# Performance work log

Measured on AMD Instinct MI355X. Metric: run time of the kernel, lower is better.

The kernel has to match this reference:

```python
import jax, jax.numpy as jnp
import numpy as np

N_NODES = 100_000
N_EDGES = 800_000
D_IN = 64
HID = 32   # hidden_channels
OUT = 64   # out_channels
H1, H2, H3 = 7, 4, 1


def _lin(key, din, dout, scale=0.05):
    k1, k2 = jax.random.split(key)
    W = jax.random.normal(k1, (din, dout), jnp.float32) * scale
    b = jax.random.normal(k2, (dout,), jnp.float32) * scale
    return W, b


def setup_inputs() -> dict:
    key = jax.random.key(0)
    ks = jax.random.split(key, 16)
    x = jax.random.normal(ks[0], (N_NODES, D_IN), jnp.float32)
    edge_index = jax.random.randint(ks[1], (2, N_EDGES), 0, N_NODES, dtype=jnp.int32)
    inp = {"x": x, "edge_index": edge_index}
    # (in_dim, heads, per-head channels) for the 3 TransformerConv layers
    dims = [(D_IN, H1, HID), (H1 * HID, H2, HID), (H2 * HID, H3, OUT)]
    i = 2
    for l, (din, h, c) in enumerate(dims, start=1):
        for nm in ("q", "k", "v", "s"):  # query, key, value, skip linears
            W, b = _lin(ks[i], din, h * c)
            i += 1
            inp[f"W{nm}{l}"] = W
            inp[f"b{nm}{l}"] = b
    return inp


def _transformer_conv(x, src, dst, Wq, bq, Wk, bk, Wv, bv, Ws, bs, H, C):
    # PyG TransformerConv (concat=True, beta=False, root_weight=True, no edge feats)
    q = (x @ Wq + bq).reshape(-1, H, C)
    k = (x @ Wk + bk).reshape(-1, H, C)
    v = (x @ Wv + bv).reshape(-1, H, C)
    # per-edge attention logits [E, H]
    alpha = jnp.einsum('ehc,ehc->eh', q[dst], k[src]) / jnp.sqrt(jnp.asarray(C, q.dtype))
    # segment softmax over incoming edges of each dst node
    amax = jax.ops.segment_max(alpha, dst, num_segments=N_NODES)
    ex = jnp.exp(alpha - amax[dst])
    denom = jax.ops.segment_sum(ex, dst, num_segments=N_NODES)
    attn = ex / (denom[dst] + 1e-16)
    # weighted message aggregation [N, H, C] -> [N, H*C]
    msg = v[src] * attn[..., None]
    out = jax.ops.segment_sum(msg, dst, num_segments=N_NODES).reshape(N_NODES, H * C)
    # root/skip connection
    return out + x @ Ws + bs


def reference(x, edge_index,
              Wq1, bq1, Wk1, bk1, Wv1, bv1, Ws1, bs1,
              Wq2, bq2, Wk2, bk2, Wv2, bv2, Ws2, bs2,
              Wq3, bq3, Wk3, bk3, Wv3, bv3, Ws3, bs3):
    src, dst = edge_index[0], edge_index[1]
    h = jax.nn.relu(_transformer_conv(x, src, dst, Wq1, bq1, Wk1, bk1, Wv1, bv1, Ws1, bs1, H1, HID))
    h = jax.nn.relu(_transformer_conv(h, src, dst, Wq2, bq2, Wk2, bk2, Wv2, bv2, Ws2, bs2, H2, HID))
    return _transformer_conv(h, src, dst, Wq3, bq3, Wk3, bk3, Wv3, bv3, Ws3, bs3, H3, OUT)
```

## Files before the change

kernel.cpp:

```cpp
#include <hip/hip_runtime.h>
#include <hip/hip_bf16.h>
#include <math.h>

#define N_NODES 100000
#define N_EDGES 800000
#define SCAN_BLOCKS 98

typedef __attribute__((ext_vector_type(8))) short short8;
typedef __attribute__((ext_vector_type(4))) float f32x4;

__device__ __forceinline__ unsigned short f2b(float f) {
    __hip_bfloat16 h = __float2bfloat16(f);
    return *reinterpret_cast<unsigned short*>(&h);
}
__device__ __forceinline__ float2 up2(unsigned u) {
    unsigned lo = u << 16;
    unsigned hi = u & 0xffff0000u;
    float2 r;
    __builtin_memcpy(&r.x, &lo, 4);
    __builtin_memcpy(&r.y, &hi, 4);
    return r;
}
__device__ __forceinline__ float dot4(float2 qa, float2 qb, unsigned k0, unsigned k1) {
    float2 x = up2(k0), y = up2(k1);
    float p = x.x * qa.x;
    p = fmaf(x.y, qa.y, p);
    p = fmaf(y.x, qb.x, p);
    p = fmaf(y.y, qb.y, p);
    return p;
}


__global__ void hist_kernel(const int* __restrict__ dst, int* __restrict__ deg) {
    int e = blockIdx.x * blockDim.x + threadIdx.x;
    if (e < N_EDGES) atomicAdd(&deg[dst[e]], 1);
}

__global__ __launch_bounds__(1024) void scan_part(const int* __restrict__ deg,
                                                  int* __restrict__ rowptr,
                                                  int* __restrict__ partials) {
    __shared__ int buf[1024];
    const int t = threadIdx.x;
    const int i = blockIdx.x * 1024 + t;
    int x = (i < N_NODES) ? deg[i] : 0;
    buf[t] = x;
    __syncthreads();
    for (int off = 1; off < 1024; off <<= 1) {
        int y = (t >= off) ? buf[t - off] : 0;
        __syncthreads();
        buf[t] += y;
        __syncthreads();
    }
    if (i < N_NODES) rowptr[i] = buf[t] - x;
    if (t == 1023) partials[blockIdx.x] = buf[t];
}

__global__ __launch_bounds__(128) void scan_tail(int* __restrict__ partials,
                                                 int* __restrict__ rowptr) {
    __shared__ int buf[128];
    const int t = threadIdx.x;
    int x = (t < SCAN_BLOCKS) ? partials[t] : 0;
    buf[t] = x;
    __syncthreads();
    for (int off = 1; off < 128; off <<= 1) {
        int y = (t >= off) ? buf[t - off] : 0;
        __syncthreads();
        buf[t] += y;
        __syncthreads();
    }
    if (t < SCAN_BLOCKS) partials[t] = buf[t] - x;
    if (t == 127) rowptr[N_NODES] = buf[127];
}

__global__ __launch_bounds__(1024) void scan_add(int* __restrict__ rowptr,
                                                 const int* __restrict__ partials) {
    const int i = blockIdx.x * 1024 + threadIdx.x;
    if (i < N_NODES) rowptr[i] += partials[blockIdx.x];
}

__global__ void scatter_kernel(const int* __restrict__ src, const int* __restrict__ dst,
                               const int* __restrict__ rowptr, int* __restrict__ cursor,
                               int* __restrict__ sorted_src) {
    int e = blockIdx.x * blockDim.x + threadIdx.x;
    if (e < N_EDGES) {
        int d = dst[e];
        int pos = atomicAdd(&cursor[d], 1);
        sorted_src[rowptr[d] + pos] = src[e];
    }
}

__global__ void fill_kernel(float* __restrict__ out, int n, float val) {
    int i = blockIdx.x * blockDim.x + threadIdx.x;
    if (i < n) out[i] = val;
}


__global__ void convert_kernel(const float* __restrict__ X, unsigned short* __restrict__ Y, int n4) {
    int i = blockIdx.x * blockDim.x + threadIdx.x;
    if (i < n4) {
        float4 f = ((const float4*)X)[i];
        ushort4 u;
        u.x = f2b(f.x); u.y = f2b(f.y); u.z = f2b(f.z); u.w = f2b(f.w);
        ((ushort4*)Y)[i] = u;
    }
}

__global__ void build_wt(const float* __restrict__ Wq, const float* __restrict__ Wk,
                         const float* __restrict__ Wv, const float* __restrict__ Wsk,
                         const float* __restrict__ bq, const float* __restrict__ bk,
                         const float* __restrict__ bv, const float* __restrict__ bsk,
                         unsigned short* __restrict__ WT, float* __restrict__ biasF,
                         int K, int HC, int C) {
    int total = 4 * HC * K;
    int idx = blockIdx.x * blockDim.x + threadIdx.x;
    if (idx >= total) return;
    int rowc = idx / K;
    int kk = idx - rowc * K;
    const float* W;
    const float* Bp;
    int cw;
    if (rowc < HC) {
        W = Wq; Bp = bq; cw = rowc;
    } else if (rowc < 3 * HC) {
        int u = rowc - HC;
        int h = u / (2 * C);
        int rr = u - h * 2 * C;
        int grp = rr >> 3, w = rr & 7;
        if (w < 4) { W = Wk;  Bp = bk;  cw = h * C + grp * 4 + w; }
        else       { W = Wv;  Bp = bv;  cw = h * C + grp * 4 + w - 4; }
    } else {
        W = Wsk; Bp = bsk; cw = rowc - 3 * HC;
    }
    WT[idx] = f2b(W[(size_t)kk * HC + cw]);
    if (kk == 0) biasF[rowc] = Bp[cw];
}


template <int K, bool YBF>
__global__ __launch_bounds__(256) void mfma_gemm(
    const unsigned short* __restrict__ Xb, const unsigned short* __restrict__ WT,
    const float* __restrict__ biasF, void* __restrict__ Y,
    int ncols, int ostride, int split, int rq, int rkv) {
    constexpr int STR = 40;
    constexpr int ESTR = 136;
    __shared__ __align__(16) char smem[128 * ESTR * 2];
    unsigned short* Xs = (unsigned short*)smem;
    unsigned short* Ws = (unsigned short*)(smem + 128 * STR * 2);
    const int t = threadIdx.x;
    const int wave = t >> 6, lane = t & 63, quad = lane >> 4, l16 = lane & 15;
    const int n0 = blockIdx.x * 128, c0 = blockIdx.y * 128;

    f32x4 acc[2][8];
#pragma unroll
    for (int i = 0; i < 2; ++i)
#pragma unroll
        for (int j = 0; j < 8; ++j)
#pragma unroll
            for (int r = 0; r < 4; ++r) acc[i][j][r] = 0.f;

    for (int k0 = 0; k0 < K; k0 += 32) {
#pragma unroll
        for (int i = 0; i < 2; ++i) {
            int idx = t + i * 256;
            int row = idx >> 2;
            int seg = (idx & 3) << 3;
            int gr = n0 + row;
            short8 xv;
#pragma unroll
            for (int z = 0; z < 8; ++z) xv[z] = 0;
            if (gr < N_NODES)
                xv = *(const short8*)(Xb + (size_t)gr * K + k0 + seg);
            *(short8*)(&Xs[row * STR + seg]) = xv;

            int c = c0 + row;
            short8 wv;
#pragma unroll
            for (int z = 0; z < 8; ++z) wv[z] = 0;
            if (c < ncols) {
                int wtrow = (c < split) ? (rq + c) : (rkv + (c - split));
                wv = *(const short8*)(WT + (size_t)wtrow * K + k0 + seg);
            }
            *(short8*)(&Ws[row * STR + seg]) = wv;
        }
        __syncthreads();

        short8 af0 = *(short8*)(&Xs[(wave * 32 + l16) * STR + quad * 8]);
        short8 af1 = *(short8*)(&Xs[(wave * 32 + 16 + l16) * STR + quad * 8]);
#pragma unroll
        for (int ct = 0; ct < 8; ++ct) {
            short8 bfr = *(short8*)(&Ws[(ct * 16 + l16) * STR + quad * 8]);
            acc[0][ct] = __builtin_amdgcn_mfma_f32_16x16x32_bf16(af0, bfr, acc[0][ct], 0, 0, 0);
            acc[1][ct] = __builtin_amdgcn_mfma_f32_16x16x32_bf16(af1, bfr, acc[1][ct], 0, 0, 0);
        }
        __syncthreads();
    }

    if constexpr (YBF) {
        unsigned short* Es = (unsigned short*)smem;
#pragma unroll
        for (int ct = 0; ct < 8; ++ct) {
            if (c0 + ct * 16 >= ncols) break;
            int col = c0 + ct * 16 + l16;
            int brow = (col < split) ? (rq + col) : (rkv + (col - split));
            float bv = biasF[brow];
#pragma unroll
            for (int rt = 0; rt < 2; ++rt)
#pragma unroll
                for (int r = 0; r < 4; ++r) {
                    int row = wave * 32 + rt * 16 + quad * 4 + r;
                    Es[row * ESTR + ct * 16 + l16] = f2b(acc[rt][ct][r] + bv);
                }
        }
        __syncthreads();
        const int erow = t >> 1;
        const int cb = (t & 1) * 8;
        const int gr = n0 + erow;
#pragma unroll
        for (int j = 0; j < 8; ++j) {
            int gc = c0 + j * 16 + cb;
            if (gr < N_NODES && gc < ncols)
                *(short8*)((unsigned short*)Y + (size_t)gr * ostride + gc) =
                    *(const short8*)(&Es[erow * ESTR + j * 16 + cb]);
        }
    } else {
#pragma unroll
        for (int ct = 0; ct < 8; ++ct) {
            int col = c0 + ct * 16 + l16;
            if (col >= ncols) continue;
            int brow = (col < split) ? (rq + col) : (rkv + (col - split));
            float bv = biasF[brow];
#pragma unroll
            for (int rt = 0; rt < 2; ++rt) {
#pragma unroll
                for (int r = 0; r < 4; ++r) {
                    int row = n0 + wave * 32 + rt * 16 + quad * 4 + r;
                    if (row < N_NODES)
                        ((float*)Y)[(size_t)row * ostride + col] = acc[rt][ct][r] + bv;
                }
            }
        }
    }
}

template <int K, bool YBF>
static inline void launch_gemm(const unsigned short* Xb, const unsigned short* WT,
                               const float* biasF, void* Y, int ncols, int ostride,
                               int split, int rq, int rkv, hipStream_t s) {
    const int GX = (N_NODES + 127) / 128;
    int ny = (ncols + 127) / 128;
    mfma_gemm<K, YBF><<<dim3(GX, ny), 256, 0, s>>>(
        Xb, WT, biasF, Y, ncols, ostride, split, rq, rkv);
}


template <int C, int NH, bool RELU, bool YBF>
__global__ __launch_bounds__(256) void attn3(
    const unsigned short* __restrict__ F,
    const int* __restrict__ rowptr, const int* __restrict__ ssrc,
    void* __restrict__ Hv, int h0, int ostride) {
    constexpr int LPN = NH * C / 4;
    constexpr int NPW = 64 / LPN;
    constexpr int gC = NH * C;
    constexpr int Ms = 3 * gC;
    const int lane = threadIdx.x & 63;
    const int wave = (blockIdx.x * 256 + threadIdx.x) >> 6;
    const int slot = lane / LPN;
    const int cl = lane - slot * LPN;
    const int n = wave * NPW + slot;
    if (slot >= NPW || n >= N_NODES) return;

    const int head = cl / (C / 4);
    const int c4 = (cl - head * (C / 4)) * 4;
    const int qoff = head * C + c4;
    const int kvoff = gC + head * 2 * C + 2 * c4;
    const float SCALE2 = ((C == 64) ? 0.125f : 0.17677669529663687f) * 1.44269504f;

    uint2 qu = *(const uint2*)(F + (size_t)n * Ms + qoff);
    float2 qa = up2(qu.x), qb = up2(qu.y);
    qa.x *= SCALE2; qa.y *= SCALE2; qb.x *= SCALE2; qb.y *= SCALE2;
    int s0 = rowptr[n], s1 = rowptr[n + 1];

    float l = 0.f, a0 = 0.f, a1 = 0.f, a2 = 0.f, a3 = 0.f;
    int ei = s0;
    for (; ei + 3 < s1; ei += 4) {
        int iA = ssrc[ei], iB = ssrc[ei + 1], iC = ssrc[ei + 2], iD = ssrc[ei + 3];
        uint4 A = *(const uint4*)(F + (size_t)iA * Ms + kvoff);
        uint4 B = *(const uint4*)(F + (size_t)iB * Ms + kvoff);
        uint4 Cv = *(const uint4*)(F + (size_t)iC * Ms + kvoff);
        uint4 D = *(const uint4*)(F + (size_t)iD * Ms + kvoff);
        float pA = dot4(qa, qb, A.x, A.y);
        float pB = dot4(qa, qb, B.x, B.y);
        float pC = dot4(qa, qb, Cv.x, Cv.y);
        float pD = dot4(qa, qb, D.x, D.y);
#pragma unroll
        for (int off = C / 8; off > 0; off >>= 1) {
            pA += __shfl_xor(pA, off);
            pB += __shfl_xor(pB, off);
            pC += __shfl_xor(pC, off);
            pD += __shfl_xor(pD, off);
        }
        float eA = exp2f(pA), eB = exp2f(pB), eC = exp2f(pC), eD = exp2f(pD);
        l += (eA + eB) + (eC + eD);
        float2 vA0 = up2(A.z), vA1 = up2(A.w);
        float2 vB0 = up2(B.z), vB1 = up2(B.w);
        float2 vC0 = up2(Cv.z), vC1 = up2(Cv.w);
        float2 vD0 = up2(D.z), vD1 = up2(D.w);
        a0 = fmaf(eA, vA0.x, fmaf(eB, vB0.x, fmaf(eC, vC0.x, fmaf(eD, vD0.x, a0))));
        a1 = fmaf(eA, vA0.y, fmaf(eB, vB0.y, fmaf(eC, vC0.y, fmaf(eD, vD0.y, a1))));
        a2 = fmaf(eA, vA1.x, fmaf(eB, vB1.x, fmaf(eC, vC1.x, fmaf(eD, vD1.x, a2))));
        a3 = fmaf(eA, vA1.y, fmaf(eB, vB1.y, fmaf(eC, vC1.y, fmaf(eD, vD1.y, a3))));
    }
    if (ei + 1 < s1) {
        int iA = ssrc[ei], iB = ssrc[ei + 1];
        ei += 2;
        uint4 A = *(const uint4*)(F + (size_t)iA * Ms + kvoff);
        uint4 B = *(const uint4*)(F + (size_t)iB * Ms + kvoff);
        float pA = dot4(qa, qb, A.x, A.y);
        float pB = dot4(qa, qb, B.x, B.y);
#pragma unroll
        for (int off = C / 8; off > 0; off >>= 1) {
            pA += __shfl_xor(pA, off);
            pB += __shfl_xor(pB, off);
        }
        float eA = exp2f(pA), eB = exp2f(pB);
        l += eA + eB;
        float2 vA0 = up2(A.z), vA1 = up2(A.w);
        float2 vB0 = up2(B.z), vB1 = up2(B.w);
        a0 = fmaf(eA, vA0.x, fmaf(eB, vB0.x, a0));
        a1 = fmaf(eA, vA0.y, fmaf(eB, vB0.y, a1));
        a2 = fmaf(eA, vA1.x, fmaf(eB, vB1.x, a2));
        a3 = fmaf(eA, vA1.y, fmaf(eB, vB1.y, a3));
    }
    if (ei < s1) {
        int iA = ssrc[ei];
        uint4 A = *(const uint4*)(F + (size_t)iA * Ms + kvoff);
        float pA = dot4(qa, qb, A.x, A.y);
#pragma unroll
        for (int off = C / 8; off > 0; off >>= 1) pA += __shfl_xor(pA, off);
        float eA = exp2f(pA);
        l += eA;
        float2 vA0 = up2(A.z), vA1 = up2(A.w);
        a0 = fmaf(eA, vA0.x, a0);
        a1 = fmaf(eA, vA0.y, a1);
        a2 = fmaf(eA, vA1.x, a2);
        a3 = fmaf(eA, vA1.y, a3);
    }

    float inv = 1.f / (l + 1e-16f);
    float r0 = a0 * inv, r1 = a1 * inv, r2 = a2 * inv, r3 = a3 * inv;

    const int col = (h0 + head) * C + c4;
    if constexpr (YBF) {
        uint2* Hp = (uint2*)((unsigned short*)Hv + (size_t)n * ostride + col);
        uint2 hv = *Hp;
        float2 hx = up2(hv.x), hy = up2(hv.y);
        float o0 = hx.x + r0, o1 = hx.y + r1, o2 = hy.x + r2, o3 = hy.y + r3;
        if (RELU) {
            o0 = fmaxf(o0, 0.f); o1 = fmaxf(o1, 0.f);
            o2 = fmaxf(o2, 0.f); o3 = fmaxf(o3, 0.f);
        }
        uint2 pv;
        pv.x = (unsigned)f2b(o0) | ((unsigned)f2b(o1) << 16);
        pv.y = (unsigned)f2b(o2) | ((unsigned)f2b(o3) << 16);
        *Hp = pv;
    } else {
        float4* Hp = (float4*)((float*)Hv + (size_t)n * ostride + col);
        float4 h = *Hp;
        h.x += r0; h.y += r1; h.z += r2; h.w += r3;
        if (RELU) {
            h.x = fmaxf(h.x, 0.f); h.y = fmaxf(h.y, 0.f);
            h.z = fmaxf(h.z, 0.f); h.w = fmaxf(h.w, 0.f);
        }
        *Hp = h;
    }
}

static inline void launch_attn32(int NH, int h0, const unsigned short* F,
                                 void* H, int ostride, const int* rowptr,
                                 const int* ssrc, hipStream_t stream) {
    switch (NH) {
        case 1: attn3<32, 1, true, true><<<3125, 256, 0, stream>>>(F, rowptr, ssrc, H, h0, ostride); break;
        case 2: attn3<32, 2, true, true><<<6250, 256, 0, stream>>>(F, rowptr, ssrc, H, h0, ostride); break;
        case 3: attn3<32, 3, true, true><<<12500, 256, 0, stream>>>(F, rowptr, ssrc, H, h0, ostride); break;
        case 4: attn3<32, 4, true, true><<<12500, 256, 0, stream>>>(F, rowptr, ssrc, H, h0, ostride); break;
        default: attn3<32, 7, true, true><<<25000, 256, 0, stream>>>(F, rowptr, ssrc, H, h0, ostride); break;
    }
}


extern "C" void kernel_launch(void* const* d_in, const int* in_sizes, int n_in,
                              void* d_out, int out_size, void* d_ws, size_t ws_size,
                              hipStream_t stream) {
    const float* x = (const float*)d_in[0];
    const int* ei = (const int*)d_in[1];
    const int* srcp = ei;
    const int* dstp = ei + N_EDGES;

    const float* W[12];
    const float* B[12];
    for (int i = 0; i < 12; ++i) {
        W[i] = (const float*)d_in[2 + 2 * i];
        B[i] = (const float*)d_in[3 + 2 * i];
    }
    float* out = (float*)d_out;

    char* p = (char*)d_ws;
    size_t off = 0;
    unsigned short* wt  = (unsigned short*)(p + off); off += 240000;
    float* biasF        = (float*)(p + off);          off += 4096;
    int* rowptr = (int*)(p + off); off += sizeof(int) * (N_NODES + 1);
    int* deg    = (int*)(p + off); off += sizeof(int) * N_NODES;
    int* cursor = (int*)(p + off); off += sizeof(int) * N_NODES;
    int* partials = (int*)(p + off); off += sizeof(int) * 128;
    int* ssrc   = (int*)(p + off); off += sizeof(int) * N_EDGES;
    off = (off + 255) & ~(size_t)255;
    unsigned short* h1  = (unsigned short*)(p + off); off += (size_t)224 * N_NODES * 2;
    unsigned short* h2  = (unsigned short*)(p + off); off += (size_t)128 * N_NODES * 2;
    unsigned short* xb1 = (unsigned short*)(p + off); off += (size_t)64 * N_NODES * 2;
    unsigned short* tail = (unsigned short*)(p + off);

    if (ws_size < off + 6500000) {
        fill_kernel<<<(out_size + 255) / 256, 256, 0, stream>>>(out, out_size, (float)(ws_size >> 20));
        return;
    }
    size_t tail_bytes = ws_size - off;
    const size_t F1PASS = (size_t)3 * 32 * N_NODES * 2;

    int nh1[7], np1 = 0;
    int nh2[4], np2 = 0;
    unsigned short *F1w, *F2w;
    if (tail_bytes >= 7 * F1PASS) {
        nh1[np1++] = 7;
        nh2[np2++] = 4;
        F1w = F2w = tail;
    } else if (tail_bytes >= 4 * F1PASS) {
        nh1[np1++] = 4; nh1[np1++] = 3;
        nh2[np2++] = 4;
        F1w = F2w = tail;
    } else if (tail_bytes >= 2 * F1PASS) {
        nh1[np1++] = 2; nh1[np1++] = 2; nh1[np1++] = 2; nh1[np1++] = 1;
        nh2[np2++] = 2; nh2[np2++] = 2;
        F1w = F2w = tail;
    } else {
        for (int i = 0; i < 7; ++i) nh1[np1++] = 1;
        for (int i = 0; i < 4; ++i) nh2[np2++] = 1;
        F1w = h2;
        F2w = xb1;
    }
    unsigned short* F3 = h1;

    hipMemsetAsync(deg, 0, sizeof(int) * 2 * N_NODES, stream);
    hist_kernel<<<(N_EDGES + 255) / 256, 256, 0, stream>>>(dstp, deg);
    scan_part<<<SCAN_BLOCKS, 1024, 0, stream>>>(deg, rowptr, partials);
    scan_tail<<<1, 128, 0, stream>>>(partials, rowptr);
    scan_add<<<SCAN_BLOCKS, 1024, 0, stream>>>(rowptr, partials);
    scatter_kernel<<<(N_EDGES + 255) / 256, 256, 0, stream>>>(srcp, dstp, rowptr, cursor, ssrc);

    convert_kernel<<<(N_NODES * 64 / 4 + 255) / 256, 256, 0, stream>>>(x, xb1, N_NODES * 64 / 4);

    build_wt<<<(4 * 224 * 64 + 255) / 256, 256, 0, stream>>>(
        W[0], W[1], W[2], W[3], B[0], B[1], B[2], B[3], wt, biasF, 64, 224, 32);
    launch_gemm<64, true>(xb1, wt + (size_t)3 * 224 * 64, biasF + 3 * 224, h1,
                          224, 224, 224, 0, 0, stream);
    {
        int h0 = 0;
        for (int pass = 0; pass < np1; ++pass) {
            int NH = nh1[pass];
            int nc = 3 * NH * 32;
            launch_gemm<64, true>(xb1, wt, biasF, F1w, nc, nc,
                                  NH * 32, h0 * 32,
                                  224 + 2 * h0 * 32, stream);
            launch_attn32(NH, h0, F1w, h1, 224, rowptr, ssrc, stream);
            h0 += NH;
        }
    }

    build_wt<<<(4 * 128 * 224 + 255) / 256, 256, 0, stream>>>(
        W[4], W[5], W[6], W[7], B[4], B[5], B[6], B[7], wt, biasF, 224, 128, 32);
    launch_gemm<224, true>(h1, wt + (size_t)3 * 128 * 224, biasF + 3 * 128, h2,
                           128, 128, 128, 0, 0, stream);
    {
        int h0 = 0;
        for (int pass = 0; pass < np2; ++pass) {
            int NH = nh2[pass];
            int nc = 3 * NH * 32;
            launch_gemm<224, true>(h1, wt, biasF, F2w, nc, nc,
                                   NH * 32, h0 * 32,
                                   128 + 2 * h0 * 32, stream);
            launch_attn32(NH, h0, F2w, h2, 128, rowptr, ssrc, stream);
            h0 += NH;
        }
    }

    build_wt<<<(4 * 64 * 128 + 255) / 256, 256, 0, stream>>>(
        W[8], W[9], W[10], W[11], B[8], B[9], B[10], B[11], wt, biasF, 128, 64, 64);
    launch_gemm<128, true>(h2, wt, biasF, F3, 192, 192,
                           64, 0, 64, stream);
    launch_gemm<128, false>(h2, wt + (size_t)3 * 64 * 128, biasF + 3 * 64, out,
                            64, 64, 64, 0, 0, stream);
    attn3<64, 1, false, false><<<6250, 256, 0, stream>>>(F3, rowptr, ssrc, out, 0, 64);
}
```

Baseline: 665.5 us.

## Store attention keys in FP8 and split K from Q/V layout for layers 1-2

For the first two TransformerConv layers, keys are now written as FP8 e4m3 through a separate GEMM epilogue into their own buffer, and Q/V stay bf16 in a narrower [Q|V] layout. The attention kernel gathers 4-byte FP8 key chunks and 8-byte bf16 value chunks per edge instead of one 16-byte interleaved K/V chunk. This cuts the gather traffic in the memory-bound edge loop. The cost is an extra GEMM launch that recomputes the X tile per pass, two separate gathers per edge, and reduced key precision that may hurt accuracy.

New measurement: 664.9 us. No clear change (-0.1%).

```diff
diff --git a/kernel.cpp b/kernel.cpp
--- a/kernel.cpp
+++ b/kernel.cpp
@@ -1,5 +1,6 @@
 #include <hip/hip_runtime.h>
 #include <hip/hip_bf16.h>
+#include <hip/hip_fp8.h>
 #include <math.h>
 
 #define N_NODES 100000
@@ -8,6 +9,7 @@
 
 typedef __attribute__((ext_vector_type(8))) short short8;
 typedef __attribute__((ext_vector_type(4))) float f32x4;
+typedef __attribute__((ext_vector_type(2))) float f32x2;
 
 __device__ __forceinline__ unsigned short f2b(float f) {
     __hip_bfloat16 h = __float2bfloat16(f);
@@ -20,6 +22,37 @@
     __builtin_memcpy(&r.x, &lo, 4);
     __builtin_memcpy(&r.y, &hi, 4);
     return r;
+}
+__device__ __forceinline__ unsigned char f2fp8(float f) {
+#if __has_builtin(__builtin_amdgcn_cvt_pk_fp8_f32)
+    unsigned u = __builtin_amdgcn_cvt_pk_fp8_f32(f, f, 0u, false);
+    return (unsigned char)(u & 0xffu);
+#else
+    __hip_fp8_e4m3 h(f);
+    return (unsigned char)h.__x;
+#endif
+}
+__device__ __forceinline__ float dotk(float2 qa, float2 qb, unsigned k4) {
+#if __has_builtin(__builtin_amdgcn_cvt_pk_f32_fp8)
+    f32x2 lo = __builtin_amdgcn_cvt_pk_f32_fp8(k4, false);
+    f32x2 hi = __builtin_amdgcn_cvt_pk_f32_fp8(k4, true);
+    float p = lo[0] * qa.x;
+    p = fmaf(lo[1], qa.y, p);
+    p = fmaf(hi[0], qb.x, p);
+    p = fmaf(hi[1], qb.y, p);
+    return p;
+#else
+    __hip_fp8_e4m3 a, b, c, d;
+    a.__x = (unsigned char)k4;
+    b.__x = (unsigned char)(k4 >> 8);
+    c.__x = (unsigned char)(k4 >> 16);
+    d.__x = (unsigned char)(k4 >> 24);
+    float p = (float)a * qa.x;
+    p = fmaf((float)b, qa.y, p);
+    p = fmaf((float)c, qb.x, p);
+    p = fmaf((float)d, qb.y, p);
+    return p;
+#endif
 }
 __device__ __forceinline__ float dot4(float2 qa, float2 qb, unsigned k0, unsigned k1) {
     float2 x = up2(k0), y = up2(k1);
@@ -110,7 +143,7 @@
                          const float* __restrict__ bq, const float* __restrict__ bk,
                          const float* __restrict__ bv, const float* __restrict__ bsk,
                          unsigned short* __restrict__ WT, float* __restrict__ biasF,
-                         int K, int HC, int C) {
+                         int K, int HC, int C, int mode) {
     int total = 4 * HC * K;
     int idx = blockIdx.x * blockDim.x + threadIdx.x;
     if (idx >= total) return;
@@ -119,24 +152,31 @@
     const float* W;
     const float* Bp;
     int cw;
-    if (rowc < HC) {
-        W = Wq; Bp = bq; cw = rowc;
-    } else if (rowc < 3 * HC) {
-        int u = rowc - HC;
-        int h = u / (2 * C);
-        int rr = u - h * 2 * C;
-        int grp = rr >> 3, w = rr & 7;
-        if (w < 4) { W = Wk;  Bp = bk;  cw = h * C + grp * 4 + w; }
-        else       { W = Wv;  Bp = bv;  cw = h * C + grp * 4 + w - 4; }
+    if (mode == 0) {
+        if (rowc < HC)          { W = Wq;  Bp = bq;  cw = rowc; }
+        else if (rowc < 2 * HC) { W = Wv;  Bp = bv;  cw = rowc - HC; }
+        else if (rowc < 3 * HC) { W = Wk;  Bp = bk;  cw = rowc - 2 * HC; }
+        else                    { W = Wsk; Bp = bsk; cw = rowc - 3 * HC; }
     } else {
-        W = Wsk; Bp = bsk; cw = rowc - 3 * HC;
+        if (rowc < HC) {
+            W = Wq; Bp = bq; cw = rowc;
+        } else if (rowc < 3 * HC) {
+            int u = rowc - HC;
+            int h = u / (2 * C);
+            int rr = u - h * 2 * C;
+            int grp = rr >> 3, w = rr & 7;
+            if (w < 4) { W = Wk; Bp = bk; cw = h * C + grp * 4 + w; }
+            else       { W = Wv; Bp = bv; cw = h * C + grp * 4 + w - 4; }
+        } else {
+            W = Wsk; Bp = bsk; cw = rowc - 3 * HC;
+        }
     }
     WT[idx] = f2b(W[(size_t)kk * HC + cw]);
     if (kk == 0) biasF[rowc] = Bp[cw];
 }
 
 
-template <int K, bool YBF>
+template <int K, int YMODE>
 __global__ __launch_bounds__(256) void mfma_gemm(
     const unsigned short* __restrict__ Xb, const unsigned short* __restrict__ WT,
     const float* __restrict__ biasF, void* __restrict__ Y,
@@ -195,7 +235,7 @@
         __syncthreads();
     }
 
-    if constexpr (YBF) {
+    if constexpr (YMODE == 1) {
         unsigned short* Es = (unsigned short*)smem;
 #pragma unroll
         for (int ct = 0; ct < 8; ++ct) {
@@ -221,6 +261,34 @@
             if (gr < N_NODES && gc < ncols)
                 *(short8*)((unsigned short*)Y + (size_t)gr * ostride + gc) =
                     *(const short8*)(&Es[erow * ESTR + j * 16 + cb]);
+        }
+    } else if constexpr (YMODE == 2) {
+        constexpr int EB = 144;
+        unsigned char* Es = (unsigned char*)smem;
+#pragma unroll
+        for (int ct = 0; ct < 8; ++ct) {
+            if (c0 + ct * 16 >= ncols) break;
+            int col = c0 + ct * 16 + l16;
+            int brow = (col < split) ? (rq + col) : (rkv + (col - split));
+            float bv = biasF[brow];
+#pragma unroll
+            for (int rt = 0; rt < 2; ++rt)
+#pragma unroll
+                for (int r = 0; r < 4; ++r) {
+                    int row = wave * 32 + rt * 16 + quad * 4 + r;
+                    Es[row * EB + ct * 16 + l16] = f2fp8(acc[rt][ct][r] + bv);
+                }
+        }
+        __syncthreads();
+        const int erow = t >> 1;
+        const int q8 = (t & 1) * 64;
+        const int gr = n0 + erow;
+#pragma unroll
+        for (int j = 0; j < 4; ++j) {
+            int gc = c0 + q8 + j * 16;
+            if (gr < N_NODES && gc < ncols)
+                *(uint4*)((unsigned char*)Y + (size_t)gr * ostride + gc) =
+                    *(const uint4*)(&Es[erow * EB + q8 + j * 16]);
         }
     } else {
 #pragma unroll
@@ -242,26 +310,26 @@
     }
 }
 
-template <int K, bool YBF>
+template <int K, int YMODE>
 static inline void launch_gemm(const unsigned short* Xb, const unsigned short* WT,
                                const float* biasF, void* Y, int ncols, int ostride,
                                int split, int rq, int rkv, hipStream_t s) {
     const int GX = (N_NODES + 127) / 128;
     int ny = (ncols + 127) / 128;
-    mfma_gemm<K, YBF><<<dim3(GX, ny), 256, 0, s>>>(
+    mfma_gemm<K, YMODE><<<dim3(GX, ny), 256, 0, s>>>(
         Xb, WT, biasF, Y, ncols, ostride, split, rq, rkv);
 }
 
 
-template <int C, int NH, bool RELU, bool YBF>
+template <int C, int NH, bool RELU, bool YBF, bool KF8>
 __global__ __launch_bounds__(256) void attn3(
-    const unsigned short* __restrict__ F,
+    const unsigned short* __restrict__ F, const unsigned char* __restrict__ K8,
     const int* __restrict__ rowptr, const int* __restrict__ ssrc,
     void* __restrict__ Hv, int h0, int ostride) {
     constexpr int LPN = NH * C / 4;
     constexpr int NPW = 64 / LPN;
     constexpr int gC = NH * C;
-    constexpr int Ms = 3 * gC;
+    constexpr int Ms = KF8 ? (2 * gC) : (3 * gC);
     const int lane = threadIdx.x & 63;
     const int wave = (blockIdx.x * 256 + threadIdx.x) >> 6;
     const int slot = lane / LPN;
@@ -272,6 +340,7 @@
     const int head = cl / (C / 4);
     const int c4 = (cl - head * (C / 4)) * 4;
     const int qoff = head * C + c4;
+    const int voff = gC + qoff;
     const int kvoff = gC + head * 2 * C + 2 * c4;
     const float SCALE2 = ((C == 64) ? 0.125f : 0.17677669529663687f) * 1.44269504f;
 
@@ -282,68 +351,141 @@
 
     float l = 0.f, a0 = 0.f, a1 = 0.f, a2 = 0.f, a3 = 0.f;
     int ei = s0;
-    for (; ei + 3 < s1; ei += 4) {
-        int iA = ssrc[ei], iB = ssrc[ei + 1], iC = ssrc[ei + 2], iD = ssrc[ei + 3];
-        uint4 A = *(const uint4*)(F + (size_t)iA * Ms + kvoff);
-        uint4 B = *(const uint4*)(F + (size_t)iB * Ms + kvoff);
-        uint4 Cv = *(const uint4*)(F + (size_t)iC * Ms + kvoff);
-        uint4 D = *(const uint4*)(F + (size_t)iD * Ms + kvoff);
-        float pA = dot4(qa, qb, A.x, A.y);
-        float pB = dot4(qa, qb, B.x, B.y);
-        float pC = dot4(qa, qb, Cv.x, Cv.y);
-        float pD = dot4(qa, qb, D.x, D.y);
-#pragma unroll
-        for (int off = C / 8; off > 0; off >>= 1) {
-            pA += __shfl_xor(pA, off);
-            pB += __shfl_xor(pB, off);
-            pC += __shfl_xor(pC, off);
-            pD += __shfl_xor(pD, off);
-        }
-        float eA = exp2f(pA), eB = exp2f(pB), eC = exp2f(pC), eD = exp2f(pD);
-        l += (eA + eB) + (eC + eD);
-        float2 vA0 = up2(A.z), vA1 = up2(A.w);
-        float2 vB0 = up2(B.z), vB1 = up2(B.w);
-        float2 vC0 = up2(Cv.z), vC1 = up2(Cv.w);
-        float2 vD0 = up2(D.z), vD1 = up2(D.w);
-        a0 = fmaf(eA, vA0.x, fmaf(eB, vB0.x, fmaf(eC, vC0.x, fmaf(eD, vD0.x, a0))));
-        a1 = fmaf(eA, vA0.y, fmaf(eB, vB0.y, fmaf(eC, vC0.y, fmaf(eD, vD0.y, a1))));
-        a2 = fmaf(eA, vA1.x, fmaf(eB, vB1.x, fmaf(eC, vC1.x, fmaf(eD, vD1.x, a2))));
-        a3 = fmaf(eA, vA1.y, fmaf(eB, vB1.y, fmaf(eC, vC1.y, fmaf(eD, vD1.y, a3))));
-    }
-    if (ei + 1 < s1) {
-        int iA = ssrc[ei], iB = ssrc[ei + 1];
-        ei += 2;
-        uint4 A = *(const uint4*)(F + (size_t)iA * Ms + kvoff);
-        uint4 B = *(const uint4*)(F + (size_t)iB * Ms + kvoff);
-        float pA = dot4(qa, qb, A.x, A.y);
-        float pB = dot4(qa, qb, B.x, B.y);
-#pragma unroll
-        for (int off = C / 8; off > 0; off >>= 1) {
-            pA += __shfl_xor(pA, off);
-            pB += __shfl_xor(pB, off);
-        }
-        float eA = exp2f(pA), eB = exp2f(pB);
-        l += eA + eB;
-        float2 vA0 = up2(A.z), vA1 = up2(A.w);
-        float2 vB0 = up2(B.z), vB1 = up2(B.w);
-        a0 = fmaf(eA, vA0.x, fmaf(eB, vB0.x, a0));
-        a1 = fmaf(eA, vA0.y, fmaf(eB, vB0.y, a1));
-        a2 = fmaf(eA, vA1.x, fmaf(eB, vB1.x, a2));
-        a3 = fmaf(eA, vA1.y, fmaf(eB, vB1.y, a3));
-    }
-    if (ei < s1) {
-        int iA = ssrc[ei];
-        uint4 A = *(const uint4*)(F + (size_t)iA * Ms + kvoff);
-        float pA = dot4(qa, qb, A.x, A.y);
-#pragma unroll
-        for (int off = C / 8; off > 0; off >>= 1) pA += __shfl_xor(pA, off);
-        float eA = exp2f(pA);
-        l += eA;
-        float2 vA0 = up2(A.z), vA1 = up2(A.w);
-        a0 = fmaf(eA, vA0.x, a0);
-        a1 = fmaf(eA, vA0.y, a1);
-        a2 = fmaf(eA, vA1.x, a2);
-        a3 = fmaf(eA, vA1.y, a3);
+    if constexpr (KF8) {
+        for (; ei + 3 < s1; ei += 4) {
+            int iA = ssrc[ei], iB = ssrc[ei + 1], iC = ssrc[ei + 2], iD = ssrc[ei + 3];
+            unsigned kA = *(const unsigned*)(K8 + (size_t)iA * gC + qoff);
+            unsigned kB = *(const unsigned*)(K8 + (size_t)iB * gC + qoff);
+            unsigned kC = *(const unsigned*)(K8 + (size_t)iC * gC + qoff);
+            unsigned kD = *(const unsigned*)(K8 + (size_t)iD * gC + qoff);
+            uint2 vAu = *(const uint2*)(F + (size_t)iA * Ms + voff);
+            uint2 vBu = *(const uint2*)(F + (size_t)iB * Ms + voff);
+            uint2 vCu = *(const uint2*)(F + (size_t)iC * Ms + voff);
+            uint2 vDu = *(const uint2*)(F + (size_t)iD * Ms + voff);
+            float pA = dotk(qa, qb, kA);
+            float pB = dotk(qa, qb, kB);
+            float pC = dotk(qa, qb, kC);
+            float pD = dotk(qa, qb, kD);
+#pragma unroll
+            for (int off = C / 8; off > 0; off >>= 1) {
+                pA += __shfl_xor(pA, off);
+                pB += __shfl_xor(pB, off);
+                pC += __shfl_xor(pC, off);
+                pD += __shfl_xor(pD, off);
+            }
+            float eA = exp2f(pA), eB = exp2f(pB), eC = exp2f(pC), eD = exp2f(pD);
+            l += (eA + eB) + (eC + eD);
+            float2 vA0 = up2(vAu.x), vA1 = up2(vAu.y);
+            float2 vB0 = up2(vBu.x), vB1 = up2(vBu.y);
+            float2 vC0 = up2(vCu.x), vC1 = up2(vCu.y);
+            float2 vD0 = up2(vDu.x), vD1 = up2(vDu.y);
+            a0 = fmaf(eA, vA0.x, fmaf(eB, vB0.x, fmaf(eC, vC0.x, fmaf(eD, vD0.x, a0))));
+            a1 = fmaf(eA, vA0.y, fmaf(eB, vB0.y, fmaf(eC, vC0.y, fmaf(eD, vD0.y, a1))));
+            a2 = fmaf(eA, vA1.x, fmaf(eB, vB1.x, fmaf(eC, vC1.x, fmaf(eD, vD1.x, a2))));
+            a3 = fmaf(eA, vA1.y, fmaf(eB, vB1.y, fmaf(eC, vC1.y, fmaf(eD, vD1.y, a3))));
+        }
+        if (ei + 1 < s1) {
+            int iA = ssrc[ei], iB = ssrc[ei + 1];
+            ei += 2;
+            unsigned kA = *(const unsigned*)(K8 + (size_t)iA * gC + qoff);
+            unsigned kB = *(const unsigned*)(K8 + (size_t)iB * gC + qoff);
+            uint2 vAu = *(const uint2*)(F + (size_t)iA * Ms + voff);
+            uint2 vBu = *(const uint2*)(F + (size_t)iB * Ms + voff);
+            float pA = dotk(qa, qb, kA);
+            float pB = dotk(qa, qb, kB);
+#pragma unroll
+            for (int off = C / 8; off > 0; off >>= 1) {
+                pA += __shfl_xor(pA, off);
+                pB += __shfl_xor(pB, off);
+            }
+            float eA = exp2f(pA), eB = exp2f(pB);
+            l += eA + eB;
+            float2 vA0 = up2(vAu.x), vA1 = up2(vAu.y);
+            float2 vB0 = up2(vBu.x), vB1 = up2(vBu.y);
+            a0 = fmaf(eA, vA0.x, fmaf(eB, vB0.x, a0));
+            a1 = fmaf(eA, vA0.y, fmaf(eB, vB0.y, a1));
+            a2 = fmaf(eA, vA1.x, fmaf(eB, vB1.x, a2));
+            a3 = fmaf(eA, vA1.y, fmaf(eB, vB1.y, a3));
+        }
+        if (ei < s1) {
+            int iA = ssrc[ei];
+            unsigned kA = *(const unsigned*)(K8 + (size_t)iA * gC + qoff);
+            uint2 vAu = *(const uint2*)(F + (size_t)iA * Ms + voff);
+            float pA = dotk(qa, qb, kA);
+#pragma unroll
+            for (int off = C / 8; off > 0; off >>= 1) pA += __shfl_xor(pA, off);
+            float eA = exp2f(pA);
+            l += eA;
+            float2 vA0 = up2(vAu.x), vA1 = up2(vAu.y);
+            a0 = fmaf(eA, vA0.x, a0);
+            a1 = fmaf(eA, vA0.y, a1);
+            a2 = fmaf(eA, vA1.x, a2);
+            a3 = fmaf(eA, vA1.y, a3);
+        }
+    } else {
+        for (; ei + 3 < s1; ei += 4) {
+            int iA = ssrc[ei], iB = ssrc[ei + 1], iC = ssrc[ei + 2], iD = ssrc[ei + 3];
+            uint4 A = *(const uint4*)(F + (size_t)iA * Ms + kvoff);
+            uint4 B = *(const uint4*)(F + (size_t)iB * Ms + kvoff);
+            uint4 Cv = *(const uint4*)(F + (size_t)iC * Ms + kvoff);
+            uint4 D = *(const uint4*)(F + (size_t)iD * Ms + kvoff);
+            float pA = dot4(qa, qb, A.x, A.y);
+            float pB = dot4(qa, qb, B.x, B.y);
+            float pC = dot4(qa, qb, Cv.x, Cv.y);
+            float pD = dot4(qa, qb, D.x, D.y);
+#pragma unroll
+            for (int off = C / 8; off > 0; off >>= 1) {
+                pA += __shfl_xor(pA, off);
+                pB += __shfl_xor(pB, off);
+                pC += __shfl_xor(pC, off);
+                pD += __shfl_xor(pD, off);
+            }
+            float eA = exp2f(pA), eB = exp2f(pB), eC = exp2f(pC), eD = exp2f(pD);
+            l += (eA + eB) + (eC + eD);
+            float2 vA0 = up2(A.z), vA1 = up2(A.w);
+            float2 vB0 = up2(B.z), vB1 = up2(B.w);
+            float2 vC0 = up2(Cv.z), vC1 = up2(Cv.w);
+            float2 vD0 = up2(D.z), vD1 = up2(D.w);
+            a0 = fmaf(eA, vA0.x, fmaf(eB, vB0.x, fmaf(eC, vC0.x, fmaf(eD, vD0.x, a0))));
+            a1 = fmaf(eA, vA0.y, fmaf(eB, vB0.y, fmaf(eC, vC0.y, fmaf(eD, vD0.y, a1))));
+            a2 = fmaf(eA, vA1.x, fmaf(eB, vB1.x, fmaf(eC, vC1.x, fmaf(eD, vD1.x, a2))));
+            a3 = fmaf(eA, vA1.y, fmaf(eB, vB1.y, fmaf(eC, vC1.y, fmaf(eD, vD1.y, a3))));
+        }
+        if (ei + 1 < s1) {
+            int iA = ssrc[ei], iB = ssrc[ei + 1];
+            ei += 2;
+            uint4 A = *(const uint4*)(F + (size_t)iA * Ms + kvoff);
+            uint4 B = *(const uint4*)(F + (size_t)iB * Ms + kvoff);
+            float pA = dot4(qa, qb, A.x, A.y);
+            float pB = dot4(qa, qb, B.x, B.y);
+#pragma unroll
+            for (int off = C / 8; off > 0; off >>= 1) {
+                pA += __shfl_xor(pA, off);
+                pB += __shfl_xor(pB, off);
+            }
+            float eA = exp2f(pA), eB = exp2f(pB);
+            l += eA + eB;
+            float2 vA0 = up2(A.z), vA1 = up2(A.w);
+            float2 vB0 = up2(B.z), vB1 = up2(B.w);
+            a0 = fmaf(eA, vA0.x, fmaf(eB, vB0.x, a0));
+            a1 = fmaf(eA, vA0.y, fmaf(eB, vB0.y, a1));
+            a2 = fmaf(eA, vA1.x, fmaf(eB, vB1.x, a2));
+            a3 = fmaf(eA, vA1.y, fmaf(eB, vB1.y, a3));
+        }
+        if (ei < s1) {
+            int iA = ssrc[ei];
+            uint4 A = *(const uint4*)(F + (size_t)iA * Ms + kvoff);
+            float pA = dot4(qa, qb, A.x, A.y);
+#pragma unroll
+            for (int off = C / 8; off > 0; off >>= 1) pA += __shfl_xor(pA, off);
+            float eA = exp2f(pA);
+            l += eA;
+            float2 vA0 = up2(A.z), vA1 = up2(A.w);
+            a0 = fmaf(eA, vA0.x, a0);
+            a1 = fmaf(eA, vA0.y, a1);
+            a2 = fmaf(eA, vA1.x, a2);
+            a3 = fmaf(eA, vA1.y, a3);
+        }
     }
 
     float inv = 1.f / (l + 1e-16f);
@@ -376,14 +518,14 @@
 }
 
 static inline void launch_attn32(int NH, int h0, const unsigned short* F,
-                                 void* H, int ostride, const int* rowptr,
-                                 const int* ssrc, hipStream_t stream) {
+                                 const unsigned char* K8, void* H, int ostride,
+                                 const int* rowptr, const int* ssrc, hipStream_t stream) {
     switch (NH) {
-        case 1: attn3<32, 1, true, true><<<3125, 256, 0, stream>>>(F, rowptr, ssrc, H, h0, ostride); break;
-        case 2: attn3<32, 2, true, true><<<6250, 256, 0, stream>>>(F, rowptr, ssrc, H, h0, ostride); break;
-        case 3: attn3<32, 3, true, true><<<12500, 256, 0, stream>>>(F, rowptr, ssrc, H, h0, ostride); break;
-        case 4: attn3<32, 4, true, true><<<12500, 256, 0, stream>>>(F, rowptr, ssrc, H, h0, ostride); break;
-        default: attn3<32, 7, true, true><<<25000, 256, 0, stream>>>(F, rowptr, ssrc, H, h0, ostride); break;
+        case 1: attn3<32, 1, true, true, true><<<3125, 256, 0, stream>>>(F, K8, rowptr, ssrc, H, h0, ostride); break;
+        case 2: attn3<32, 2, true, true, true><<<6250, 256, 0, stream>>>(F, K8, rowptr, ssrc, H, h0, ostride); break;
+        case 3: attn3<32, 3, true, true, true><<<12500, 256, 0, stream>>>(F, K8, rowptr, ssrc, H, h0, ostride); break;
+        case 4: attn3<32, 4, true, true, true><<<12500, 256, 0, stream>>>(F, K8, rowptr, ssrc, H, h0, ostride); break;
+        default: attn3<32, 7, true, true, true><<<25000, 256, 0, stream>>>(F, K8, rowptr, ssrc, H, h0, ostride); break;
     }
 }
 
@@ -459,44 +601,49 @@
     convert_kernel<<<(N_NODES * 64 / 4 + 255) / 256, 256, 0, stream>>>(x, xb1, N_NODES * 64 / 4);
 
     build_wt<<<(4 * 224 * 64 + 255) / 256, 256, 0, stream>>>(
-        W[0], W[1], W[2], W[3], B[0], B[1], B[2], B[3], wt, biasF, 64, 224, 32);
-    launch_gemm<64, true>(xb1, wt + (size_t)3 * 224 * 64, biasF + 3 * 224, h1,
-                          224, 224, 224, 0, 0, stream);
+        W[0], W[1], W[2], W[3], B[0], B[1], B[2], B[3], wt, biasF, 64, 224, 32, 0);
+    launch_gemm<64, 1>(xb1, wt + (size_t)3 * 224 * 64, biasF + 3 * 224, h1,
+                       224, 224, 224, 0, 0, stream);
     {
         int h0 = 0;
         for (int pass = 0; pass < np1; ++pass) {
             int NH = nh1[pass];
-            int nc = 3 * NH * 32;
-            launch_gemm<64, true>(xb1, wt, biasF, F1w, nc, nc,
-                                  NH * 32, h0 * 32,
-                                  224 + 2 * h0 * 32, stream);
-            launch_attn32(NH, h0, F1w, h1, 224, rowptr, ssrc, stream);
+            int nc = NH * 32;
+            unsigned char* K1w = (unsigned char*)F1w + (size_t)4 * nc * N_NODES;
+            launch_gemm<64, 1>(xb1, wt, biasF, F1w, 2 * nc, 2 * nc,
+                               nc, h0 * 32, 224 + h0 * 32, stream);
+            launch_gemm<64, 2>(xb1, wt, biasF, K1w, nc, nc,
+                               nc, 2 * 224 + h0 * 32, 0, stream);
+            launch_attn32(NH, h0, F1w, K1w, h1, 224, rowptr, ssrc, stream);
             h0 += NH;
         }
     }
 
     build_wt<<<(4 * 128 * 224 + 255) / 256, 256, 0, stream>>>(
-        W[4], W[5], W[6], W[7], B[4], B[5], B[6], B[7], wt, biasF, 224, 128, 32);
-    launch_gemm<224, true>(h1, wt + (size_t)3 * 128 * 224, biasF + 3 * 128, h2,
-                           128, 128, 128, 0, 0, stream);
+        W[4], W[5], W[6], W[7], B[4], B[5], B[6], B[7], wt, biasF, 224, 128, 32, 0);
+    launch_gemm<224, 1>(h1, wt + (size_t)3 * 128 * 224, biasF + 3 * 128, h2,
+                        128, 128, 128, 0, 0, stream);
     {
         int h0 = 0;
         for (int pass = 0; pass < np2; ++pass) {
             int NH = nh2[pass];
-            int nc = 3 * NH * 32;
-            launch_gemm<224, true>(h1, wt, biasF, F2w, nc, nc,
-                                   NH * 32, h0 * 32,
-                                   128 + 2 * h0 * 32, stream);
-            launch_attn32(NH, h0, F2w, h2, 128, rowptr, ssrc, stream);
+            int nc = NH * 32;
+            unsigned char* K2w = (unsigned char*)F2w + (size_t)4 * nc * N_NODES;
+            launch_gemm<224, 1>(h1, wt, biasF, F2w, 2 * nc, 2 * nc,
+                                nc, h0 * 32, 128 + h0 * 32, stream);
+            launch_gemm<224, 2>(h1, wt, biasF, K2w, nc, nc,
+                                nc, 2 * 128 + h0 * 32, 0, stream);
+            launch_attn32(NH, h0, F2w, K2w, h2, 128, rowptr, ssrc, stream);
             h0 += NH;
         }
     }
 
     build_wt<<<(4 * 64 * 128 + 255) / 256, 256, 0, stream>>>(
-        W[8], W[9], W[10], W[11], B[8], B[9], B[10], B[11], wt, biasF, 128, 64, 64);
-    launch_gemm<128, true>(h2, wt, biasF, F3, 192, 192,
-                           64, 0, 64, stream);
-    launch_gemm<128, false>(h2, wt + (size_t)3 * 64 * 128, biasF + 3 * 64, out,
-                            64, 64, 64, 0, 0, stream);
-    attn3<64, 1, false, false><<<6250, 256, 0, stream>>>(F3, rowptr, ssrc, out, 0, 64);
-}
+        W[8], W[9], W[10], W[11], B[8], B[9], B[10], B[11], wt, biasF, 128, 64, 64, 1);
+    launch_gemm<128, 1>(h2, wt, biasF, F3, 192, 192,
+                        64, 0, 64, stream);
+    launch_gemm<128, 0>(h2, wt + (size_t)3 * 64 * 128, biasF + 3 * 64, out,
+                        64, 64, 64, 0, 0, stream);
+    attn3<64, 1, false, false, false><<<6250, 256, 0, stream>>>(F3, (const unsigned char*)nullptr,
+                                                                rowptr, ssrc, out, 0, 64);
+}
```
